# Kernel tuning notes

Hardware: AMD Instinct MI355X
Metric: run time of the kernel (lower is better)

The kernel has to match this reference:

```python
import jax, jax.numpy as jnp
import numpy as np

NUM_GRAPHS = 64

def _sage(x_src, x_dst, ei, Wl, bl, Wr):
    # PyG SAGEConv (aggr='mean', root_weight=True): lin_l(mean_j x_j) + lin_r(x_dst)
    src, dst = ei[0], ei[1]
    n_dst = x_dst.shape[0]
    msg = jnp.take(x_src, src, axis=0)                      # [E, D] gather
    s = jax.ops.segment_sum(msg, dst, num_segments=n_dst)   # [N_dst, D] scatter-add
    deg = jax.ops.segment_sum(jnp.ones(src.shape, x_src.dtype), dst, num_segments=n_dst)
    mean = s / jnp.maximum(deg, 1.0)[:, None]
    return (mean @ Wl + bl) + x_dst @ Wr

def _mean_pool(x, batch):
    s = jax.ops.segment_sum(x, batch, num_segments=NUM_GRAPHS)
    c = jax.ops.segment_sum(jnp.ones((x.shape[0],), x.dtype), batch, num_segments=NUM_GRAPHS)
    return s / jnp.maximum(c, 1.0)[:, None]

def setup_inputs() -> dict:
    key = jax.random.key(0)
    ks = jax.random.split(key, 40)
    N, E, D, H, C = 50000, 1600000, 128, 128, 2
    inp = {}
    inp['x_user'] = jax.random.normal(ks[0], (N, D), jnp.float32)
    inp['x_drug'] = jax.random.normal(ks[1], (N, D), jnp.float32)
    inp['ei_ud'] = jax.random.randint(ks[2], (2, E), 0, N)
    inp['ei_du'] = jax.random.randint(ks[3], (2, E), 0, N)
    inp['ei_uu'] = jax.random.randint(ks[4], (2, E), 0, N)
    inp['batch_user'] = jnp.sort(jax.random.randint(ks[5], (N,), 0, NUM_GRAPHS))
    inp['batch_drug'] = jnp.sort(jax.random.randint(ks[6], (N,), 0, NUM_GRAPHS))
    i = 7
    for lyr in (1, 2):
        for et in ('ud', 'du', 'uu'):
            inp[f'Wl{lyr}_{et}'] = jax.random.normal(ks[i], (D, H), jnp.float32) / np.float32(np.sqrt(D)); i += 1
            inp[f'bl{lyr}_{et}'] = jnp.zeros((H,), jnp.float32)
            inp[f'Wr{lyr}_{et}'] = jax.random.normal(ks[i], (D, H), jnp.float32) / np.float32(np.sqrt(D)); i += 1
    inp['W1'] = jax.random.normal(ks[i], (2 * H, H), jnp.float32) / np.float32(np.sqrt(2 * H)); i += 1
    inp['b1'] = jnp.zeros((H,), jnp.float32)
    inp['W2'] = jax.random.normal(ks[i], (H, C), jnp.float32) / np.float32(np.sqrt(H)); i += 1
    inp['b2'] = jnp.zeros((C,), jnp.float32)
    return inp

def reference(x_user, x_drug, ei_ud, ei_du, ei_uu, batch_user, batch_drug,
              Wl1_ud, bl1_ud, Wr1_ud, Wl1_du, bl1_du, Wr1_du, Wl1_uu, bl1_uu, Wr1_uu,
              Wl2_ud, bl2_ud, Wr2_ud, Wl2_du, bl2_du, Wr2_du, Wl2_uu, bl2_uu, Wr2_uu,
              W1, b1, W2, b2):
    # Layer 1 (HeteroConv sums per-dst-type contributions), then ReLU
    u1 = _sage(x_drug, x_user, ei_du, Wl1_du, bl1_du, Wr1_du) \
       + _sage(x_user, x_user, ei_uu, Wl1_uu, bl1_uu, Wr1_uu)
    d1 = _sage(x_user, x_drug, ei_ud, Wl1_ud, bl1_ud, Wr1_ud)
    u1 = jax.nn.relu(u1)
    d1 = jax.nn.relu(d1)
    # Layer 2 (no ReLU in original before pooling)
    u2 = _sage(d1, u1, ei_du, Wl2_du, bl2_du, Wr2_du) \
       + _sage(u1, u1, ei_uu, Wl2_uu, bl2_uu, Wr2_uu)
    d2 = _sage(u1, d1, ei_ud, Wl2_ud, bl2_ud, Wr2_ud)
    # Per-node-type global mean pool, concat along feature dim
    x_pool = jnp.concatenate([_mean_pool(u2, batch_user), _mean_pool(d2, batch_drug)], axis=1)
    h = jax.nn.relu(x_pool @ W1 + b1)
    logits = h @ W2 + b2
    return jax.nn.log_softmax(logits, axis=1)
```

## Files before the change

kernel.cpp:

```cpp
#include <hip/hip_runtime.h>

#define NG 64
#define REP 8
#define GSC 512
#define NBK_MAX 1024

typedef __bf16 bf16x8 __attribute__((ext_vector_type(8)));
typedef float  f32x4  __attribute__((ext_vector_type(4)));
typedef float  f32x2  __attribute__((ext_vector_type(2)));

__device__ __forceinline__ ushort f2bf(float f) {
    unsigned int b = __float_as_uint(f);
    b += 0x7fffu + ((b >> 16) & 1u);
    return (ushort)(b >> 16);
}

__device__ __forceinline__ f32x2 fp8pair(unsigned w) {
    return __builtin_amdgcn_cvt_pk_f32_fp8((int)w, false);
}
__device__ __forceinline__ unsigned fp8enc2(float a, float b) {
    return (unsigned)__builtin_amdgcn_cvt_pk_fp8_f32(a, b, 0, false) & 0xffffu;
}
__device__ __forceinline__ unsigned char fp8enc1(float a) {
    return (unsigned char)(__builtin_amdgcn_cvt_pk_fp8_f32(a, 0.f, 0, false) & 0xff);
}

__global__ __launch_bounds__(256) void bucket_count3(
    const int* __restrict__ d0, int E0, int nbk0, int* __restrict__ c0,
    const int* __restrict__ d1, int E1, int nbk1, int* __restrict__ c1,
    const int* __restrict__ d2, int E2, int nbk2, int* __restrict__ c2)
{
    const int* dst; int E, nbk; int* cntA;
    if (blockIdx.y == 0) { dst = d0; E = E0; nbk = nbk0; cntA = c0; }
    else if (blockIdx.y == 1) { dst = d1; E = E1; nbk = nbk1; cntA = c1; }
    else { dst = d2; E = E2; nbk = nbk2; cntA = c2; }
    __shared__ int h[NBK_MAX];
    for (int i = threadIdx.x; i < nbk; i += 256) h[i] = 0;
    __syncthreads();
    int chunk = (E + GSC - 1) / GSC;
    int i0 = blockIdx.x * chunk, i1 = min(E, i0 + chunk);
    for (int i = i0 + threadIdx.x; i < i1; i += 256)
        atomicAdd(&h[dst[i] >> 6], 1);
    __syncthreads();
    for (int i = threadIdx.x; i < nbk; i += 256)
        cntA[(size_t)i * GSC + blockIdx.x] = h[i];
}

__global__ __launch_bounds__(GSC) void scan_blocks3(
    int* __restrict__ c0, int nbk0, int* __restrict__ bt0,
    int* __restrict__ c1, int nbk1, int* __restrict__ bt1,
    int* __restrict__ c2, int nbk2, int* __restrict__ bt2)
{
    int* cntA; int nbk; int* btot;
    if (blockIdx.y == 0) { cntA = c0; nbk = nbk0; btot = bt0; }
    else if (blockIdx.y == 1) { cntA = c1; nbk = nbk1; btot = bt1; }
    else { cntA = c2; nbk = nbk2; btot = bt2; }
    int b = blockIdx.x;
    if (b >= nbk) return;
    int t = threadIdx.x, lane = t & 63, wv = t >> 6;
    __shared__ int wsum[8];
    int v = cntA[(size_t)b * GSC + t];
    int x = v;
    #pragma unroll
    for (int off = 1; off < 64; off <<= 1) { int u = __shfl_up(x, off, 64); if (lane >= off) x += u; }
    if (lane == 63) wsum[wv] = x;
    __syncthreads();
    if (wv == 0 && lane < 8) {
        int w = wsum[lane];
        #pragma unroll
        for (int off = 1; off < 8; off <<= 1) { int u = __shfl_up(w, off, 64); if (lane >= off) w += u; }
        wsum[lane] = w;
    }
    __syncthreads();
    int incl = x + (wv > 0 ? wsum[wv - 1] : 0);
    cntA[(size_t)b * GSC + t] = incl - v;
    if (t == GSC - 1) btot[b] = incl;
}

__global__ __launch_bounds__(1024) void scan_buckets3(
    const int* __restrict__ bt0, int nbk0, int* __restrict__ bb0,
    const int* __restrict__ bt1, int nbk1, int* __restrict__ bb1,
    const int* __restrict__ bt2, int nbk2, int* __restrict__ bb2)
{
    const int* btot; int nbk; int* bbase;
    if (blockIdx.x == 0) { btot = bt0; nbk = nbk0; bbase = bb0; }
    else if (blockIdx.x == 1) { btot = bt1; nbk = nbk1; bbase = bb1; }
    else { btot = bt2; nbk = nbk2; bbase = bb2; }
    int t = threadIdx.x, lane = t & 63, wv = t >> 6;
    __shared__ int wsum[16];
    int v = (t < nbk) ? btot[t] : 0;
    int x = v;
    #pragma unroll
    for (int off = 1; off < 64; off <<= 1) { int u = __shfl_up(x, off, 64); if (lane >= off) x += u; }
    if (lane == 63) wsum[wv] = x;
    __syncthreads();
    if (wv == 0 && lane < 16) {
        int w = wsum[lane];
        #pragma unroll
        for (int off = 1; off < 16; off <<= 1) { int u = __shfl_up(w, off, 64); if (lane >= off) w += u; }
        wsum[lane] = w;
    }
    __syncthreads();
    int incl = x + (wv > 0 ? wsum[wv - 1] : 0);
    if (t <= nbk) bbase[t] = incl - v;
}

__global__ __launch_bounds__(256) void bucket_scatter3(
    const int* __restrict__ s0, const int* __restrict__ d0, int E0, int nbk0,
    const int* __restrict__ ba0, const int* __restrict__ bb0, int2* __restrict__ eb0,
    const int* __restrict__ s1, const int* __restrict__ d1, int E1, int nbk1,
    const int* __restrict__ ba1, const int* __restrict__ bb1, int2* __restrict__ eb1,
    const int* __restrict__ s2, const int* __restrict__ d2, int E2, int nbk2,
    const int* __restrict__ ba2, const int* __restrict__ bb2, int2* __restrict__ eb2)
{
    const int *src, *dst, *basesA, *bbase; int E, nbk; int2* ebuf;
    if (blockIdx.y == 0) { src = s0; dst = d0; E = E0; nbk = nbk0; basesA = ba0; bbase = bb0; ebuf = eb0; }
    else if (blockIdx.y == 1) { src = s1; dst = d1; E = E1; nbk = nbk1; basesA = ba1; bbase = bb1; ebuf = eb1; }
    else { src = s2; dst = d2; E = E2; nbk = nbk2; basesA = ba2; bbase = bb2; ebuf = eb2; }
    __shared__ int cur[NBK_MAX];
    for (int i = threadIdx.x; i < nbk; i += 256)
        cur[i] = bbase[i] + basesA[(size_t)i * GSC + blockIdx.x];
    __syncthreads();
    int chunk = (E + GSC - 1) / GSC;
    int i0 = blockIdx.x * chunk, i1 = min(E, i0 + chunk);
    for (int i = i0 + threadIdx.x; i < i1; i += 256) {
        int d = dst[i];
        int pos = atomicAdd(&cur[d >> 6], 1);
        ebuf[pos] = make_int2(src[i], d);
    }
}

__global__ __launch_bounds__(256) void csrify3(
    const int2* __restrict__ eb0, const int* __restrict__ bb0, int M0, int E0, int nbk0,
    int* __restrict__ rp0, int* __restrict__ cs0,
    const int2* __restrict__ eb1, const int* __restrict__ bb1, int M1, int E1, int nbk1,
    int* __restrict__ rp1, int* __restrict__ cs1,
    const int2* __restrict__ eb2, const int* __restrict__ bb2, int M2, int E2, int nbk2,
    int* __restrict__ rp2, int* __restrict__ cs2)
{
    const int2* ebuf; const int* bbase; int M, E, nbk; int *rp, *csr;
    if (blockIdx.y == 0) { ebuf = eb0; bbase = bb0; M = M0; E = E0; nbk = nbk0; rp = rp0; csr = cs0; }
    else if (blockIdx.y == 1) { ebuf = eb1; bbase = bb1; M = M1; E = E1; nbk = nbk1; rp = rp1; csr = cs1; }
    else { ebuf = eb2; bbase = bb2; M = M2; E = E2; nbk = nbk2; rp = rp2; csr = cs2; }
    if ((int)blockIdx.x >= nbk) return;
    __shared__ int hist[64], cur[64];
    int t = threadIdx.x;
    if (t < 64) hist[t] = 0;
    __syncthreads();
    int e0 = bbase[blockIdx.x], e1 = bbase[blockIdx.x + 1];
    for (int e = e0 + t; e < e1; e += 256)
        atomicAdd(&hist[ebuf[e].y & 63], 1);
    __syncthreads();
    if (t < 64) {
        int x = hist[t];
        #pragma unroll
        for (int off = 1; off < 64; off <<= 1) { int u = __shfl_up(x, off, 64); if (t >= off) x += u; }
        int ex = x - hist[t];
        cur[t] = ex;
        int row = (blockIdx.x << 6) + t;
        if (row < M) rp[row] = e0 + ex;
    }
    if (blockIdx.x == 0 && t == 0) rp[M] = E;
    __syncthreads();
    for (int e = e0 + t; e < e1; e += 256) {
        int2 p = ebuf[e];
        int pos = atomicAdd(&cur[p.y & 63], 1);
        csr[e0 + pos] = p.x;
    }
}

__global__ void add2_kernel(const float* __restrict__ a, const float* __restrict__ b,
                            float* __restrict__ o, int n) {
    int i = blockIdx.x * blockDim.x + threadIdx.x;
    if (i < n) o[i] = a[i] + b[i];
}

__global__ void cvt_dual_kernel(const float* __restrict__ x, ushort* __restrict__ ob,
                                unsigned char* __restrict__ o8, int n4) {
    int i = blockIdx.x * blockDim.x + threadIdx.x;
    if (i >= n4) return;
    float4 v = ((const float4*)x)[i];
    ushort4 rb;
    rb.x = f2bf(v.x); rb.y = f2bf(v.y); rb.z = f2bf(v.z); rb.w = f2bf(v.w);
    ((ushort4*)ob)[i] = rb;
    unsigned lo = fp8enc2(v.x, v.y);
    unsigned hi = fp8enc2(v.z, v.w);
    ((unsigned int*)o8)[i] = lo | (hi << 16);
}

__global__ void wprep_kernel(
    const float* __restrict__ Wa0, const float* __restrict__ Wb0, ushort* __restrict__ Wt0,
    const float* __restrict__ Wa1, ushort* __restrict__ Wt1,
    const float* __restrict__ Wa2, ushort* __restrict__ Wt2,
    const float* __restrict__ Wa3, ushort* __restrict__ Wt3,
    const float* __restrict__ Wa4, ushort* __restrict__ Wt4)
{
    const float* Wa; const float* Wb = nullptr; ushort* Wt;
    switch (blockIdx.x) {
        case 0: Wa = Wa0; Wb = Wb0; Wt = Wt0; break;
        case 1: Wa = Wa1; Wt = Wt1; break;
        case 2: Wa = Wa2; Wt = Wt2; break;
        case 3: Wa = Wa3; Wt = Wt3; break;
        default: Wa = Wa4; Wt = Wt4; break;
    }
    for (int idx = threadIdx.x; idx < 128 * 128; idx += 256) {
        int n = idx >> 7, k = idx & 127;
        float v = Wa[k * 128 + n];
        if (Wb) v += Wb[k * 128 + n];
        Wt[idx] = f2bf(v);
    }
}

__global__ void bounds_kernel(const int* __restrict__ bu, int nu,
                              const int* __restrict__ bd, int nd,
                              int* __restrict__ bndu, int* __restrict__ bndd)
{
    const int* b = blockIdx.x == 0 ? bu : bd;
    int        n = blockIdx.x == 0 ? nu : nd;
    int*       o = blockIdx.x == 0 ? bndu : bndd;
    int g = threadIdx.x;
    if (g > NG) return;
    int lo = 0, hi = n;
    while (lo < hi) { int m = (lo + hi) >> 1; if (b[m] < g) lo = m + 1; else hi = m; }
    o[g] = lo;
}

#define GATHER8(J)                                                                   \
    {                                                                                \
        ushort w0 = *(const ushort*)&xf8[(size_t)csr[(J) + 0] * 128 + lane * 2];     \
        ushort w1 = *(const ushort*)&xf8[(size_t)csr[(J) + 1] * 128 + lane * 2];     \
        ushort w2 = *(const ushort*)&xf8[(size_t)csr[(J) + 2] * 128 + lane * 2];     \
        ushort w3 = *(const ushort*)&xf8[(size_t)csr[(J) + 3] * 128 + lane * 2];     \
        ushort w4 = *(const ushort*)&xf8[(size_t)csr[(J) + 4] * 128 + lane * 2];     \
        ushort w5 = *(const ushort*)&xf8[(size_t)csr[(J) + 5] * 128 + lane * 2];     \
        ushort w6 = *(const ushort*)&xf8[(size_t)csr[(J) + 6] * 128 + lane * 2];     \
        ushort w7 = *(const ushort*)&xf8[(size_t)csr[(J) + 7] * 128 + lane * 2];     \
        f32x2 p0 = fp8pair(w0), p1 = fp8pair(w1), p2 = fp8pair(w2), p3 = fp8pair(w3);\
        f32x2 p4 = fp8pair(w4), p5 = fp8pair(w5), p6 = fp8pair(w6), p7 = fp8pair(w7);\
        sx += (p0[0] + p1[0]) + (p2[0] + p3[0]) + (p4[0] + p5[0]) + (p6[0] + p7[0]); \
        sy += (p0[1] + p1[1]) + (p2[1] + p3[1]) + (p4[1] + p5[1]) + (p6[1] + p7[1]); \
    }

__global__ __launch_bounds__(256) void agg3_kernel(
    const unsigned char* __restrict__ x0, const int* __restrict__ rpa, const int* __restrict__ csa, int Ma, ushort* __restrict__ ma,
    const unsigned char* __restrict__ x1, const int* __restrict__ rpb, const int* __restrict__ csb, int Mb, ushort* __restrict__ mb,
    const unsigned char* __restrict__ x2, const int* __restrict__ rpc, const int* __restrict__ csc, int Mc, ushort* __restrict__ mc)
{
    const unsigned char* xf8; const int *rp, *csr; int M; ushort* mean;
    if (blockIdx.y == 0) { xf8 = x0; rp = rpa; csr = csa; M = Ma; mean = ma; }
    else if (blockIdx.y == 1) { xf8 = x1; rp = rpb; csr = csb; M = Mb; mean = mb; }
    else { xf8 = x2; rp = rpc; csr = csc; M = Mc; mean = mc; }
    int wave = threadIdx.x >> 6, lane = threadIdx.x & 63;
    int row = blockIdx.x * 4 + wave;
    if (row >= M) return;
    int s0 = rp[row], s1 = rp[row + 1];
    float sx = 0.f, sy = 0.f;
    int j = s0;
    for (; j + 8 <= s1; j += 8) GATHER8(j)
    for (; j < s1; ++j) {
        ushort w = *(const ushort*)&xf8[(size_t)csr[j] * 128 + lane * 2];
        f32x2 p = fp8pair(w);
        sx += p[0]; sy += p[1];
    }
    int deg = s1 - s0;
    float sc = 1.f / (float)(deg > 1 ? deg : 1);
    unsigned int pk = (unsigned int)f2bf(sx * sc) | ((unsigned int)f2bf(sy * sc) << 16);
    *(unsigned int*)&mean[(size_t)row * 128 + lane * 2] = pk;
}

template<int NA>
__global__ __launch_bounds__(256) void gemm_mfma(
    const ushort* __restrict__ A0, const ushort* __restrict__ A1, const ushort* __restrict__ A2,
    const ushort* __restrict__ Wt0, const ushort* __restrict__ Wt1, const ushort* __restrict__ Wt2,
    int M, const float* __restrict__ bias, unsigned char* __restrict__ C)
{
    int wave = threadIdx.x >> 6, lane = threadIdx.x & 63;
    int row0 = blockIdx.x * 64 + wave * 16;
    int r  = lane & 15;
    int kg = lane >> 4;
    f32x4 acc[8];
    #pragma unroll
    for (int nt = 0; nt < 8; ++nt) acc[nt] = (f32x4){0.f, 0.f, 0.f, 0.f};

    int arow = row0 + r;
    int arow_c = arow < M ? arow : 0;
    #pragma unroll
    for (int term = 0; term < NA; ++term) {
        const ushort* A  = (term == 0) ? A0  : (term == 1 ? A1  : A2);
        const ushort* Wt = (term == 0) ? Wt0 : (term == 1 ? Wt1 : Wt2);
        #pragma unroll
        for (int kk = 0; kk < 4; ++kk) {
            bf16x8 a = *(const bf16x8*)&A[(size_t)arow_c * 128 + kk * 32 + kg * 8];
            #pragma unroll
            for (int nt = 0; nt < 8; ++nt) {
                bf16x8 b = *(const bf16x8*)&Wt[(size_t)(nt * 16 + r) * 128 + kk * 32 + kg * 8];
                acc[nt] = __builtin_amdgcn_mfma_f32_16x16x32_bf16(a, b, acc[nt], 0, 0, 0);
            }
        }
    }

    #pragma unroll
    for (int nt = 0; nt < 8; ++nt) {
        int col = nt * 16 + r;
        float bv = bias[col];
        #pragma unroll
        for (int j = 0; j < 4; ++j) {
            int orow = row0 + kg * 4 + j;
            if (orow < M) {
                float v = fmaxf(acc[nt][j] + bv, 0.f);
                C[(size_t)orow * 128 + col] = fp8enc1(v);
            }
        }
    }
}

__global__ __launch_bounds__(256) void aggpool3_kernel(
    const unsigned char* __restrict__ x0, const int* __restrict__ rpa, const int* __restrict__ csa,
    const int* __restrict__ ba, int Ma, float* __restrict__ pa,
    const unsigned char* __restrict__ x1, const int* __restrict__ rpb, const int* __restrict__ csb,
    const int* __restrict__ bb, int Mb, float* __restrict__ pb,
    const unsigned char* __restrict__ x2, const int* __restrict__ rpc, const int* __restrict__ csc,
    const int* __restrict__ bc, int Mc, float* __restrict__ pc)
{
    const unsigned char* xf8; const int *rp, *csr, *batch; int M; float* pool;
    if (blockIdx.y == 0) { xf8 = x0; rp = rpa; csr = csa; batch = ba; M = Ma; pool = pa; }
    else if (blockIdx.y == 1) { xf8 = x1; rp = rpb; csr = csb; batch = bb; M = Mb; pool = pb; }
    else { xf8 = x2; rp = rpc; csr = csc; batch = bc; M = Mc; pool = pc; }
    int wave = threadIdx.x >> 6, lane = threadIdx.x & 63;
    int r0 = (blockIdx.x * 4 + wave) * 4;
    if (r0 >= M) return;
    int r1 = min(M, r0 + 4);
    float* p = pool + (size_t)(blockIdx.x & (REP - 1)) * NG * 128;
    float ax = 0.f, ay = 0.f;
    int curg = batch[r0];
    for (int row = r0; row < r1; ++row) {
        int g = batch[row];
        if (g != curg) {
            atomicAdd(&p[curg * 128 + lane * 2],     ax);
            atomicAdd(&p[curg * 128 + lane * 2 + 1], ay);
            ax = 0.f; ay = 0.f; curg = g;
        }
        int s0 = rp[row], s1 = rp[row + 1];
        float sx = 0.f, sy = 0.f;
        int j = s0;
        for (; j + 8 <= s1; j += 8) GATHER8(j)
        for (; j < s1; ++j) {
            ushort w = *(const ushort*)&xf8[(size_t)csr[j] * 128 + lane * 2];
            f32x2 pv = fp8pair(w);
            sx += pv[0]; sy += pv[1];
        }
        int deg = s1 - s0;
        float sc = 1.f / (float)(deg > 1 ? deg : 1);
        ax += sx * sc; ay += sy * sc;
    }
    atomicAdd(&p[curg * 128 + lane * 2],     ax);
    atomicAdd(&p[curg * 128 + lane * 2 + 1], ay);
}

__global__ __launch_bounds__(256) void pool2_kernel(
    const unsigned char* __restrict__ u1f, const unsigned char* __restrict__ d1f,
    const int* __restrict__ bndu, const int* __restrict__ bndd,
    float* __restrict__ pu1, float* __restrict__ pd1)
{
    const unsigned char* xf8; const int* bnd; float* pool;
    if (blockIdx.y == 0) { xf8 = u1f; bnd = bndu; pool = pu1; }
    else { xf8 = d1f; bnd = bndd; pool = pd1; }
    int g = blockIdx.x;
    int lo = bnd[g], hi = bnd[g + 1];
    int c2 = threadIdx.x & 63, half = threadIdx.x >> 6;
    float sx = 0.f, sy = 0.f;
    for (int r = lo + half; r < hi; r += 4) {
        ushort w = *(const ushort*)&xf8[(size_t)r * 128 + c2 * 2];
        f32x2 p = fp8pair(w);
        sx += p[0]; sy += p[1];
    }
    __shared__ float ls[256 * 2];
    ls[threadIdx.x * 2]     = sx;
    ls[threadIdx.x * 2 + 1] = sy;
    __syncthreads();
    if (half == 0) {
        float ox = ls[c2 * 2] + ls[(64 + c2) * 2] + ls[(128 + c2) * 2] + ls[(192 + c2) * 2];
        float oy = ls[c2 * 2 + 1] + ls[(64 + c2) * 2 + 1] + ls[(128 + c2) * 2 + 1] + ls[(192 + c2) * 2 + 1];
        pool[g * 128 + c2 * 2]     = ox;
        pool[g * 128 + c2 * 2 + 1] = oy;
    }
}

__global__ __launch_bounds__(128) void final_kernel(
    const float* __restrict__ pmdu, const float* __restrict__ pmuu, const float* __restrict__ pmud,
    const float* __restrict__ pu1,  const float* __restrict__ pd1,
    const int* __restrict__ bndu, const int* __restrict__ bndd,
    const float* __restrict__ Wl2_du, const float* __restrict__ bl2_du, const float* __restrict__ Wr2_du,
    const float* __restrict__ Wl2_uu, const float* __restrict__ bl2_uu, const float* __restrict__ Wr2_uu,
    const float* __restrict__ Wl2_ud, const float* __restrict__ bl2_ud, const float* __restrict__ Wr2_ud,
    const float* __restrict__ W1, const float* __restrict__ b1,
    const float* __restrict__ W2, const float* __restrict__ b2,
    float* __restrict__ out)
{
    int g = blockIdx.x, t = threadIdx.x;
    __shared__ float smdu[128], smuu[128], smud[128], su1[128], sd1[128];
    __shared__ float xrow[256], h[128], lg[2];
    float vdu = 0.f, vuu = 0.f, vud = 0.f;
    #pragma unroll
    for (int r = 0; r < REP; ++r) {
        vdu += pmdu[(size_t)r * NG * 128 + g * 128 + t];
        vuu += pmuu[(size_t)r * NG * 128 + g * 128 + t];
        vud += pmud[(size_t)r * NG * 128 + g * 128 + t];
    }
    smdu[t] = vdu;
    smuu[t] = vuu;
    smud[t] = vud;
    su1[t]  = pu1[g * 128 + t];
    sd1[t]  = pd1[g * 128 + t];
    __syncthreads();
    float ncu = (float)(bndu[g + 1] - bndu[g]);
    float ncd = (float)(bndd[g + 1] - bndd[g]);
    float cu = ncu > 1.f ? ncu : 1.f, cd = ncd > 1.f ? ncd : 1.f;
    float accu = ncu * (bl2_du[t] + bl2_uu[t]);
    float accd = ncd * bl2_ud[t];
    for (int k = 0; k < 128; ++k) {
        accu += smdu[k] * Wl2_du[k * 128 + t]
              + smuu[k] * Wl2_uu[k * 128 + t]
              + su1[k]  * (Wr2_du[k * 128 + t] + Wr2_uu[k * 128 + t]);
        accd += smud[k] * Wl2_ud[k * 128 + t]
              + sd1[k]  * Wr2_ud[k * 128 + t];
    }
    xrow[t]       = accu / cu;
    xrow[128 + t] = accd / cd;
    __syncthreads();
    float hh = b1[t];
    for (int k = 0; k < 256; ++k) hh += xrow[k] * W1[k * 128 + t];
    h[t] = fmaxf(hh, 0.f);
    __syncthreads();
    if (t < 2) {
        float l = b2[t];
        for (int k = 0; k < 128; ++k) l += h[k] * W2[k * 2 + t];
        lg[t] = l;
    }
    __syncthreads();
    if (t == 0) {
        float m = fmaxf(lg[0], lg[1]);
        float lse = m + logf(expf(lg[0] - m) + expf(lg[1] - m));
        out[g * 2 + 0] = lg[0] - lse;
        out[g * 2 + 1] = lg[1] - lse;
    }
}

extern "C" void kernel_launch(void* const* d_in, const int* in_sizes, int n_in,
                              void* d_out, int out_size, void* d_ws, size_t ws_size,
                              hipStream_t stream)
{
    const float* x_user = (const float*)d_in[0];
    const float* x_drug = (const float*)d_in[1];
    const int* ei_ud = (const int*)d_in[2];
    const int* ei_du = (const int*)d_in[3];
    const int* ei_uu = (const int*)d_in[4];
    const int* batch_u = (const int*)d_in[5];
    const int* batch_d = (const int*)d_in[6];
    const float* Wl1_ud = (const float*)d_in[7];  const float* bl1_ud = (const float*)d_in[8];  const float* Wr1_ud = (const float*)d_in[9];
    const float* Wl1_du = (const float*)d_in[10]; const float* bl1_du = (const float*)d_in[11]; const float* Wr1_du = (const float*)d_in[12];
    const float* Wl1_uu = (const float*)d_in[13]; const float* bl1_uu = (const float*)d_in[14]; const float* Wr1_uu = (const float*)d_in[15];
    const float* Wl2_ud = (const float*)d_in[16]; const float* bl2_ud = (const float*)d_in[17]; const float* Wr2_ud = (const float*)d_in[18];
    const float* Wl2_du = (const float*)d_in[19]; const float* bl2_du = (const float*)d_in[20]; const float* Wr2_du = (const float*)d_in[21];
    const float* Wl2_uu = (const float*)d_in[22]; const float* bl2_uu = (const float*)d_in[23]; const float* Wr2_uu = (const float*)d_in[24];
    const float* W1 = (const float*)d_in[25]; const float* b1 = (const float*)d_in[26];
    const float* W2 = (const float*)d_in[27]; const float* b2 = (const float*)d_in[28];
    (void)n_in; (void)out_size; (void)ws_size;

    const int Nu = in_sizes[0] / 128;
    const int Nd = in_sizes[1] / 128;
    const int E_ud = in_sizes[2] / 2;
    const int E_du = in_sizes[3] / 2;
    const int E_uu = in_sizes[4] / 2;
    const int nbk_u = (Nu + 63) >> 6;
    const int nbk_d = (Nd + 63) >> 6;
    const int nbk_max = nbk_u > nbk_d ? nbk_u : nbk_d;
    const int Nmax = Nu > Nd ? Nu : Nd;

    char* ws = (char*)d_ws;
    size_t off = 0;
    auto alloc = [&](size_t bytes) -> void* {
        void* p = ws + off;
        off = (off + bytes + 255) & ~(size_t)255;
        return p;
    };
    int2* ebuf_ud = (int2*)alloc((size_t)E_ud * 8);
    int2* ebuf_du = (int2*)alloc((size_t)E_du * 8);
    int2* ebuf_uu = (int2*)alloc((size_t)E_uu * 8);
    int* cntA_ud = (int*)alloc((size_t)NBK_MAX * GSC * 4);
    int* cntA_du = (int*)alloc((size_t)NBK_MAX * GSC * 4);
    int* cntA_uu = (int*)alloc((size_t)NBK_MAX * GSC * 4);
    int* btot_ud = (int*)alloc((size_t)NBK_MAX * 4);
    int* btot_du = (int*)alloc((size_t)NBK_MAX * 4);
    int* btot_uu = (int*)alloc((size_t)NBK_MAX * 4);
    int* bbase_ud = (int*)alloc((size_t)(NBK_MAX + 1) * 4);
    int* bbase_du = (int*)alloc((size_t)(NBK_MAX + 1) * 4);
    int* bbase_uu = (int*)alloc((size_t)(NBK_MAX + 1) * 4);
    int* csr_ud = (int*)alloc((size_t)E_ud * 4);
    int* csr_du = (int*)alloc((size_t)E_du * 4);
    int* csr_uu = (int*)alloc((size_t)E_uu * 4);
    int* rp_ud = (int*)alloc((size_t)(Nd + 1) * 4);
    int* rp_du = (int*)alloc((size_t)(Nu + 1) * 4);
    int* rp_uu = (int*)alloc((size_t)(Nu + 1) * 4);
    ushort* xb_u = (ushort*)alloc((size_t)Nu * 128 * 2);
    ushort* xb_d = (ushort*)alloc((size_t)Nd * 128 * 2);
    unsigned char* xf8_u = (unsigned char*)alloc((size_t)Nu * 128);
    unsigned char* xf8_d = (unsigned char*)alloc((size_t)Nd * 128);
    ushort* mean_du = (ushort*)ebuf_du;
    ushort* mean_uu = (ushort*)ebuf_uu;
    ushort* mean_ud = (ushort*)ebuf_ud;
    unsigned char* u1f = (unsigned char*)alloc((size_t)Nu * 128);
    unsigned char* d1f = (unsigned char*)alloc((size_t)Nd * 128);
    float* pmdu = (float*)alloc((size_t)REP * NG * 128 * 4);
    float* pmuu = (float*)alloc((size_t)REP * NG * 128 * 4);
    float* pmud = (float*)alloc((size_t)REP * NG * 128 * 4);
    char* zero2_beg = (char*)pmdu;
    char* zero2_end = ws + off;
    float* pu1  = (float*)alloc(NG * 128 * 4);
    float* pd1  = (float*)alloc(NG * 128 * 4);
    int* bnd_u = (int*)alloc((NG + 1) * 4);
    int* bnd_d = (int*)alloc((NG + 1) * 4);
    ushort* Wt_ru  = (ushort*)alloc(128 * 128 * 2);
    ushort* Wt_ldu = (ushort*)alloc(128 * 128 * 2);
    ushort* Wt_luu = (ushort*)alloc(128 * 128 * 2);
    ushort* Wt_rud = (ushort*)alloc(128 * 128 * 2);
    ushort* Wt_lud = (ushort*)alloc(128 * 128 * 2);
    float* b1s_u  = (float*)alloc(128 * 4);

    const int* dst_ud = ei_ud + E_ud;
    const int* dst_du = ei_du + E_du;
    const int* dst_uu = ei_uu + E_uu;

    bucket_count3<<<dim3(GSC, 3), 256, 0, stream>>>(
        dst_ud, E_ud, nbk_d, cntA_ud,
        dst_du, E_du, nbk_u, cntA_du,
        dst_uu, E_uu, nbk_u, cntA_uu);
    scan_blocks3<<<dim3(nbk_max, 3), GSC, 0, stream>>>(
        cntA_ud, nbk_d, btot_ud,
        cntA_du, nbk_u, btot_du,
        cntA_uu, nbk_u, btot_uu);
    scan_buckets3<<<3, 1024, 0, stream>>>(
        btot_ud, nbk_d, bbase_ud,
        btot_du, nbk_u, bbase_du,
        btot_uu, nbk_u, bbase_uu);
    bucket_scatter3<<<dim3(GSC, 3), 256, 0, stream>>>(
        ei_ud, dst_ud, E_ud, nbk_d, cntA_ud, bbase_ud, ebuf_ud,
        ei_du, dst_du, E_du, nbk_u, cntA_du, bbase_du, ebuf_du,
        ei_uu, dst_uu, E_uu, nbk_u, cntA_uu, bbase_uu, ebuf_uu);
    csrify3<<<dim3(nbk_max, 3), 256, 0, stream>>>(
        ebuf_ud, bbase_ud, Nd, E_ud, nbk_d, rp_ud, csr_ud,
        ebuf_du, bbase_du, Nu, E_du, nbk_u, rp_du, csr_du,
        ebuf_uu, bbase_uu, Nu, E_uu, nbk_u, rp_uu, csr_uu);

    bounds_kernel<<<2, NG + 1, 0, stream>>>(batch_u, Nu, batch_d, Nd, bnd_u, bnd_d);
    cvt_dual_kernel<<<(Nu * 32 + 255) / 256, 256, 0, stream>>>(x_user, xb_u, xf8_u, Nu * 32);
    cvt_dual_kernel<<<(Nd * 32 + 255) / 256, 256, 0, stream>>>(x_drug, xb_d, xf8_d, Nd * 32);
    wprep_kernel<<<5, 256, 0, stream>>>(Wr1_du, Wr1_uu, Wt_ru,
                                        Wl1_du, Wt_ldu, Wl1_uu, Wt_luu,
                                        Wr1_ud, Wt_rud, Wl1_ud, Wt_lud);
    add2_kernel<<<1, 128, 0, stream>>>(bl1_du, bl1_uu, b1s_u, 128);
    hipMemsetAsync(zero2_beg, 0, (size_t)(zero2_end - zero2_beg), stream);

    agg3_kernel<<<dim3((Nmax + 3) / 4, 3), 256, 0, stream>>>(
        xf8_d, rp_du, csr_du, Nu, mean_du,
        xf8_u, rp_uu, csr_uu, Nu, mean_uu,
        xf8_u, rp_ud, csr_ud, Nd, mean_ud);

    gemm_mfma<3><<<(Nu + 63) / 64, 256, 0, stream>>>(xb_u, mean_du, mean_uu,
                                                     Wt_ru, Wt_ldu, Wt_luu, Nu, b1s_u, u1f);
    gemm_mfma<2><<<(Nd + 63) / 64, 256, 0, stream>>>(xb_d, mean_ud, nullptr,
                                                     Wt_rud, Wt_lud, nullptr, Nd, bl1_ud, d1f);

    aggpool3_kernel<<<dim3((Nmax + 15) / 16, 3), 256, 0, stream>>>(
        d1f, rp_du, csr_du, batch_u, Nu, pmdu,
        u1f, rp_uu, csr_uu, batch_u, Nu, pmuu,
        u1f, rp_ud, csr_ud, batch_d, Nd, pmud);

    pool2_kernel<<<dim3(NG, 2), 256, 0, stream>>>(u1f, d1f, bnd_u, bnd_d, pu1, pd1);

    final_kernel<<<NG, 128, 0, stream>>>(pmdu, pmuu, pmud, pu1, pd1, bnd_u, bnd_d,
                                         Wl2_du, bl2_du, Wr2_du,
                                         Wl2_uu, bl2_uu, Wr2_uu,
                                         Wl2_ud, bl2_ud, Wr2_ud,
                                         W1, b1, W2, b2, (float*)d_out);
}
```

Baseline: 577.4 us.

## Merge small prep kernels into one launch and vectorize CSR index loads

Merges the weight transpose/convert, bias add and graph-bounds kernels into a single 7-block prep kernel, and the two feature conversion kernels into one 2D-grid launch, cutting kernel launch count. The gather macro now loads its eight neighbour indices as two int4 vector loads instead of eight scalar loads, and the CSR buffers are padded by 8 entries so reads past the end stay in bounds. The int4 loads need 16-byte alignment, which only holds if the gather offset J is always a multiple of 4; otherwise the result is misaligned access.

```diff
diff --git a/kernel.cpp b/kernel.cpp
--- a/kernel.cpp
+++ b/kernel.cpp
@@ -169,14 +169,54 @@
     }
 }
 
-__global__ void add2_kernel(const float* __restrict__ a, const float* __restrict__ b,
-                            float* __restrict__ o, int n) {
-    int i = blockIdx.x * blockDim.x + threadIdx.x;
-    if (i < n) o[i] = a[i] + b[i];
-}
-
-__global__ void cvt_dual_kernel(const float* __restrict__ x, ushort* __restrict__ ob,
-                                unsigned char* __restrict__ o8, int n4) {
+__global__ __launch_bounds__(256) void prep_kernel(
+    const float* __restrict__ Wa0, const float* __restrict__ Wb0, ushort* __restrict__ Wt0,
+    const float* __restrict__ Wa1, ushort* __restrict__ Wt1,
+    const float* __restrict__ Wa2, ushort* __restrict__ Wt2,
+    const float* __restrict__ Wa3, ushort* __restrict__ Wt3,
+    const float* __restrict__ Wa4, ushort* __restrict__ Wt4,
+    const float* __restrict__ ba, const float* __restrict__ bb, float* __restrict__ bo,
+    const int* __restrict__ bu, int nu, const int* __restrict__ bd, int nd,
+    int* __restrict__ bndu, int* __restrict__ bndd)
+{
+    if (blockIdx.x < 5) {
+        const float* Wa; const float* Wb = nullptr; ushort* Wt;
+        switch (blockIdx.x) {
+            case 0: Wa = Wa0; Wb = Wb0; Wt = Wt0; break;
+            case 1: Wa = Wa1; Wt = Wt1; break;
+            case 2: Wa = Wa2; Wt = Wt2; break;
+            case 3: Wa = Wa3; Wt = Wt3; break;
+            default: Wa = Wa4; Wt = Wt4; break;
+        }
+        for (int idx = threadIdx.x; idx < 128 * 128; idx += 256) {
+            int n = idx >> 7, k = idx & 127;
+            float v = Wa[k * 128 + n];
+            if (Wb) v += Wb[k * 128 + n];
+            Wt[idx] = f2bf(v);
+        }
+    } else if (blockIdx.x == 5) {
+        int t = threadIdx.x;
+        if (t < 128) bo[t] = ba[t] + bb[t];
+    } else {
+        int g = threadIdx.x & 127, which = threadIdx.x >> 7;
+        if (g > NG) return;
+        const int* b = which == 0 ? bu : bd;
+        int        n = which == 0 ? nu : nd;
+        int*       o = which == 0 ? bndu : bndd;
+        int lo = 0, hi = n;
+        while (lo < hi) { int m = (lo + hi) >> 1; if (b[m] < g) lo = m + 1; else hi = m; }
+        o[g] = lo;
+    }
+}
+
+__global__ void cvt_dual2_kernel(const float* __restrict__ xu, ushort* __restrict__ obu,
+                                 unsigned char* __restrict__ o8u, int n4u,
+                                 const float* __restrict__ xd, ushort* __restrict__ obd,
+                                 unsigned char* __restrict__ o8d, int n4d)
+{
+    const float* x; ushort* ob; unsigned char* o8; int n4;
+    if (blockIdx.y == 0) { x = xu; ob = obu; o8 = o8u; n4 = n4u; }
+    else { x = xd; ob = obd; o8 = o8d; n4 = n4d; }
     int i = blockIdx.x * blockDim.x + threadIdx.x;
     if (i >= n4) return;
     float4 v = ((const float4*)x)[i];
@@ -188,53 +228,18 @@
     ((unsigned int*)o8)[i] = lo | (hi << 16);
 }
 
-__global__ void wprep_kernel(
-    const float* __restrict__ Wa0, const float* __restrict__ Wb0, ushort* __restrict__ Wt0,
-    const float* __restrict__ Wa1, ushort* __restrict__ Wt1,
-    const float* __restrict__ Wa2, ushort* __restrict__ Wt2,
-    const float* __restrict__ Wa3, ushort* __restrict__ Wt3,
-    const float* __restrict__ Wa4, ushort* __restrict__ Wt4)
-{
-    const float* Wa; const float* Wb = nullptr; ushort* Wt;
-    switch (blockIdx.x) {
-        case 0: Wa = Wa0; Wb = Wb0; Wt = Wt0; break;
-        case 1: Wa = Wa1; Wt = Wt1; break;
-        case 2: Wa = Wa2; Wt = Wt2; break;
-        case 3: Wa = Wa3; Wt = Wt3; break;
-        default: Wa = Wa4; Wt = Wt4; break;
-    }
-    for (int idx = threadIdx.x; idx < 128 * 128; idx += 256) {
-        int n = idx >> 7, k = idx & 127;
-        float v = Wa[k * 128 + n];
-        if (Wb) v += Wb[k * 128 + n];
-        Wt[idx] = f2bf(v);
-    }
-}
-
-__global__ void bounds_kernel(const int* __restrict__ bu, int nu,
-                              const int* __restrict__ bd, int nd,
-                              int* __restrict__ bndu, int* __restrict__ bndd)
-{
-    const int* b = blockIdx.x == 0 ? bu : bd;
-    int        n = blockIdx.x == 0 ? nu : nd;
-    int*       o = blockIdx.x == 0 ? bndu : bndd;
-    int g = threadIdx.x;
-    if (g > NG) return;
-    int lo = 0, hi = n;
-    while (lo < hi) { int m = (lo + hi) >> 1; if (b[m] < g) lo = m + 1; else hi = m; }
-    o[g] = lo;
-}
-
 #define GATHER8(J)                                                                   \
     {                                                                                \
-        ushort w0 = *(const ushort*)&xf8[(size_t)csr[(J) + 0] * 128 + lane * 2];     \
-        ushort w1 = *(const ushort*)&xf8[(size_t)csr[(J) + 1] * 128 + lane * 2];     \
-        ushort w2 = *(const ushort*)&xf8[(size_t)csr[(J) + 2] * 128 + lane * 2];     \
-        ushort w3 = *(const ushort*)&xf8[(size_t)csr[(J) + 3] * 128 + lane * 2];     \
-        ushort w4 = *(const ushort*)&xf8[(size_t)csr[(J) + 4] * 128 + lane * 2];     \
-        ushort w5 = *(const ushort*)&xf8[(size_t)csr[(J) + 5] * 128 + lane * 2];     \
-        ushort w6 = *(const ushort*)&xf8[(size_t)csr[(J) + 6] * 128 + lane * 2];     \
-        ushort w7 = *(const ushort*)&xf8[(size_t)csr[(J) + 7] * 128 + lane * 2];     \
+        int4 ia = *(const int4*)&csr[(J)];                                           \
+        int4 ib = *(const int4*)&csr[(J) + 4];                                       \
+        ushort w0 = *(const ushort*)&xf8[(size_t)ia.x * 128 + lane * 2];             \
+        ushort w1 = *(const ushort*)&xf8[(size_t)ia.y * 128 + lane * 2];             \
+        ushort w2 = *(const ushort*)&xf8[(size_t)ia.z * 128 + lane * 2];             \
+        ushort w3 = *(const ushort*)&xf8[(size_t)ia.w * 128 + lane * 2];             \
+        ushort w4 = *(const ushort*)&xf8[(size_t)ib.x * 128 + lane * 2];             \
+        ushort w5 = *(const ushort*)&xf8[(size_t)ib.y * 128 + lane * 2];             \
+        ushort w6 = *(const ushort*)&xf8[(size_t)ib.z * 128 + lane * 2];             \
+        ushort w7 = *(const ushort*)&xf8[(size_t)ib.w * 128 + lane * 2];             \
         f32x2 p0 = fp8pair(w0), p1 = fp8pair(w1), p2 = fp8pair(w2), p3 = fp8pair(w3);\
         f32x2 p4 = fp8pair(w4), p5 = fp8pair(w5), p6 = fp8pair(w6), p7 = fp8pair(w7);\
         sx += (p0[0] + p1[0]) + (p2[0] + p3[0]) + (p4[0] + p5[0]) + (p6[0] + p7[0]); \
@@ -496,9 +501,9 @@
     int* bbase_ud = (int*)alloc((size_t)(NBK_MAX + 1) * 4);
     int* bbase_du = (int*)alloc((size_t)(NBK_MAX + 1) * 4);
     int* bbase_uu = (int*)alloc((size_t)(NBK_MAX + 1) * 4);
-    int* csr_ud = (int*)alloc((size_t)E_ud * 4);
-    int* csr_du = (int*)alloc((size_t)E_du * 4);
-    int* csr_uu = (int*)alloc((size_t)E_uu * 4);
+    int* csr_ud = (int*)alloc((size_t)(E_ud + 8) * 4);
+    int* csr_du = (int*)alloc((size_t)(E_du + 8) * 4);
+    int* csr_uu = (int*)alloc((size_t)(E_uu + 8) * 4);
     int* rp_ud = (int*)alloc((size_t)(Nd + 1) * 4);
     int* rp_du = (int*)alloc((size_t)(Nu + 1) * 4);
     int* rp_uu = (int*)alloc((size_t)(Nu + 1) * 4);
@@ -552,13 +557,14 @@
         ebuf_du, bbase_du, Nu, E_du, nbk_u, rp_du, csr_du,
         ebuf_uu, bbase_uu, Nu, E_uu, nbk_u, rp_uu, csr_uu);
 
-    bounds_kernel<<<2, NG + 1, 0, stream>>>(batch_u, Nu, batch_d, Nd, bnd_u, bnd_d);
-    cvt_dual_kernel<<<(Nu * 32 + 255) / 256, 256, 0, stream>>>(x_user, xb_u, xf8_u, Nu * 32);
-    cvt_dual_kernel<<<(Nd * 32 + 255) / 256, 256, 0, stream>>>(x_drug, xb_d, xf8_d, Nd * 32);
-    wprep_kernel<<<5, 256, 0, stream>>>(Wr1_du, Wr1_uu, Wt_ru,
-                                        Wl1_du, Wt_ldu, Wl1_uu, Wt_luu,
-                                        Wr1_ud, Wt_rud, Wl1_ud, Wt_lud);
-    add2_kernel<<<1, 128, 0, stream>>>(bl1_du, bl1_uu, b1s_u, 128);
+    prep_kernel<<<7, 256, 0, stream>>>(Wr1_du, Wr1_uu, Wt_ru,
+                                       Wl1_du, Wt_ldu, Wl1_uu, Wt_luu,
+                                       Wr1_ud, Wt_rud, Wl1_ud, Wt_lud,
+                                       bl1_du, bl1_uu, b1s_u,
+                                       batch_u, Nu, batch_d, Nd, bnd_u, bnd_d);
+    cvt_dual2_kernel<<<dim3((Nmax * 32 + 255) / 256, 2), 256, 0, stream>>>(
+        x_user, xb_u, xf8_u, Nu * 32,
+        x_drug, xb_d, xf8_d, Nd * 32);
     hipMemsetAsync(zero2_beg, 0, (size_t)(zero2_end - zero2_beg), stream);
 
     agg3_kernel<<<dim3((Nmax + 3) / 4, 3), 256, 0, stream>>>(
```

After: 567.0 us. Within noise of the previous version (-1.8%).
